# Performance work log

Measured on AMD Instinct MI355X. Metric: run time of the kernel, lower is better.

The kernel has to match this reference:

```python
import jax, jax.numpy as jnp
import numpy as np

B, L, NMOD = 200, 50, 3          # dialogues, uniform dialogue length, modalities (l,a,v)
N_DIM, NHIDDEN, NUM_K, NSPK = 128, 128, 4, 2
NN = B * NMOD * L                # total graph nodes = 30000


def _build_edge_index():
    # within-modality full permutations per dialogue
    idx = np.arange(L)
    u, v = np.meshgrid(idx, idx, indexing='ij')
    m = u != v
    pw = np.stack([u[m], v[m]])                                    # [2, L*(L-1)]
    offs = (np.arange(B)[:, None] * NMOD * L + np.arange(NMOD)[None, :] * L).reshape(-1)
    within = (pw[None, :, :] + offs[:, None, None]).transpose(1, 0, 2).reshape(2, -1)
    # cross-modal permutations of (l_t, a_t, v_t) per utterance
    mo = np.arange(NMOD) * L
    mu, mv = np.meshgrid(mo, mo, indexing='ij')
    mm = mu != mv
    pc = np.stack([mu[mm], mv[mm]])                                # [2, 6]
    offs2 = (np.arange(B)[:, None] * NMOD * L + np.arange(L)[None, :]).reshape(-1)
    cross = (pc[None, :, :] + offs2[:, None, None]).transpose(1, 0, 2).reshape(2, -1)
    return np.concatenate([within, cross], axis=1).astype(np.int32)  # [2, 1530000]


def setup_inputs():
    key = jax.random.key(0)
    ks = jax.random.split(key, 6)
    a = jax.random.normal(ks[0], (B * L, N_DIM), jnp.float32)
    v = jax.random.normal(ks[1], (B * L, N_DIM), jnp.float32)
    l = jax.random.normal(ks[2], (B * L, N_DIM), jnp.float32)
    qmask = jax.random.uniform(ks[3], (L, B, NSPK), jnp.float32)
    W1 = jax.random.normal(ks[4], (NHIDDEN, N_DIM), jnp.float32) / np.sqrt(N_DIM)
    b1 = jnp.zeros((NHIDDEN,), jnp.float32)
    speaker_emb = jax.random.normal(ks[5], (NSPK, N_DIM), jnp.float32)
    kappas = jnp.ones((NUM_K,), jnp.float32)
    edge_index = jnp.asarray(_build_edge_index())
    return {"a": a, "v": v, "l": l, "qmask": qmask, "W1": W1, "b1": b1,
            "speaker_emb": speaker_emb, "kappas": kappas,
            "edge_index": edge_index, "epoch": 0}


def _hgcn_block(x, src, dst, inv_deg, kappa):
    # gather-aggregate-scatter hypergraph conv: mean over incoming edges, kappa-weighted residual
    agg = jax.ops.segment_sum(x[src], dst, num_segments=NN) * inv_deg
    return jax.nn.relu(x + kappa * agg)


def reference(a, v, l, qmask, W1, b1, speaker_emb, kappas, edge_index, epoch):
    # flatten qmask per dialogue (uniform lengths) -> speaker id per utterance
    spk_idx = jnp.argmax(qmask.transpose(1, 0, 2).reshape(B * L, NSPK), axis=-1)
    l = l + speaker_emb[spk_idx]                    # use_speaker and 'l' in modals
    # per-dialogue node ordering: [l_b; a_b; v_b]
    feats = jnp.concatenate([l.reshape(B, L, N_DIM),
                             a.reshape(B, L, N_DIM),
                             v.reshape(B, L, N_DIM)], axis=1).reshape(NN, N_DIM)
    x = feats @ W1.T + b1
    src, dst = edge_index[0], edge_index[1]
    deg = jax.ops.segment_sum(jnp.ones((src.shape[0],), jnp.float32), dst, num_segments=NN)
    inv_deg = (1.0 / jnp.maximum(deg, 1.0))[:, None]
    for k in range(NUM_K):
        x = _hgcn_block(x, src, dst, inv_deg, kappas[k])
    x = jnp.concatenate([feats, x], axis=-1)        # use_residue
    D = x.shape[-1]
    xr = x.reshape(B, NMOD, L, D)
    # reverse_features: cat l/a/v feature blocks along last dim, utterance-major
    out = jnp.concatenate([xr[:, 0], xr[:, 1], xr[:, 2]], axis=-1).reshape(B * L, NMOD * D)
    return out
```

## Files before the change

### kernel.cpp

```cpp
#include <hip/hip_runtime.h>

#define NB   200
#define LL   50
#define ND   128

typedef __attribute__((ext_vector_type(8))) short bf16x8;
typedef __attribute__((ext_vector_type(4))) float f32x4;

#define FS   136
#define SMEM_BYTES (192 * FS * 2)

__device__ __forceinline__ short f2bf(float x) {
    unsigned u = __float_as_uint(x);
    return (short)((u + 0x7fffu + ((u >> 16) & 1u)) >> 16);
}

__device__ __forceinline__ bf16x8 pack8(f32x4 lo, f32x4 hi) {
    bf16x8 r;
    r[0] = f2bf(lo[0]); r[1] = f2bf(lo[1]); r[2] = f2bf(lo[2]); r[3] = f2bf(lo[3]);
    r[4] = f2bf(hi[0]); r[5] = f2bf(hi[1]); r[6] = f2bf(hi[2]); r[7] = f2bf(hi[3]);
    return r;
}

__launch_bounds__(1024, 4)
__global__ void hgcn_fused(const float* __restrict__ a,
                           const float* __restrict__ v,
                           const float* __restrict__ l,
                           const float* __restrict__ qmask,
                           const float* __restrict__ W1,
                           const float* __restrict__ b1,
                           const float* __restrict__ se,
                           const float* __restrict__ kap,
                           float* __restrict__ out) {
    extern __shared__ char smem[];
    short* featsB = (short*)smem;

    const int b    = blockIdx.x;
    const int tid  = threadIdx.x;
    const int lane = tid & 63;
    const int w    = tid >> 6;
    const int r    = lane & 15;
    const int q    = lane >> 4;

    const f32x4* a4  = (const f32x4*)a;
    const f32x4* v4  = (const f32x4*)v;
    const f32x4* l4  = (const f32x4*)l;
    const f32x4* se4 = (const f32x4*)se;
    const f32x4* W14 = (const f32x4*)W1;
    f32x4* out4 = (f32x4*)out;

    f32x4 kap4 = {0.f, 0.f, 0.f, 0.f};
    float bias = 0.0f;
    bf16x8 wfr[4];
    const int d = 16 * w + r;
    if (tid < 512) {
        kap4 = *(const f32x4*)kap;
        bias = b1[d];
        #pragma unroll
        for (int ks = 0; ks < 4; ++ks) {
            f32x4 g0 = W14[d * 32 + ks * 8 + q * 2];
            f32x4 g1 = W14[d * 32 + ks * 8 + q * 2 + 1];
            wfr[ks] = pack8(g0, g1);
        }
    }

    for (int i = tid; i < 3072; i += 1024) {
        int prow = i >> 4, c8 = i & 15;
        int m = prow >> 6, t = prow & 63;
        f32x4 f0 = {0.f, 0.f, 0.f, 0.f}, f1 = {0.f, 0.f, 0.f, 0.f};
        if (t < LL) {
            const f32x4* src = (m == 0) ? l4 : ((m == 1) ? a4 : v4);
            int base = (b * LL + t) * 32 + c8 * 2;
            f0 = src[base]; f1 = src[base + 1];
            if (m == 0) {
                int qb  = (t * NB + b) * 2;
                int spk = qmask[qb + 1] > qmask[qb] ? 1 : 0;
                f0 += se4[spk * 32 + c8 * 2];
                f1 += se4[spk * 32 + c8 * 2 + 1];
            }
        }
        *(bf16x8*)&featsB[prow * FS + c8 * 8] = pack8(f0, f1);
    }
    __syncthreads();

    if (tid < 512) {
        f32x4 acc[12];
        #pragma unroll
        for (int nt = 0; nt < 12; ++nt) acc[nt] = (f32x4){0.f, 0.f, 0.f, 0.f};
        #pragma unroll
        for (int ks = 0; ks < 4; ++ks)
            #pragma unroll
            for (int nt = 0; nt < 12; ++nt) {
                bf16x8 af = *(const bf16x8*)&featsB[(16 * nt + r) * FS + ks * 32 + q * 8];
                acc[nt] = __builtin_amdgcn_mfma_f32_16x16x32_bf16(af, wfr[ks], acc[nt], 0, 0, 0);
            }

        #pragma unroll
        for (int nt = 0; nt < 12; ++nt) {
            int t0 = 16 * (nt & 3) + 4 * q;
            #pragma unroll
            for (int e = 0; e < 4; ++e)
                acc[nt][e] = (t0 + e < LL) ? acc[nt][e] + bias : 0.0f;
        }

        const float inv = 1.0f / 51.0f;
        #pragma unroll
        for (int it = 0; it < 4; ++it) {
            const float f = kap4[it] * inv;
            const float g = 1.0f - 2.0f * f;
            float S[3];
            #pragma unroll
            for (int m = 0; m < 3; ++m) {
                f32x4 s4 = acc[4 * m] + acc[4 * m + 1] + acc[4 * m + 2] + acc[4 * m + 3];
                float s = s4[0] + s4[1] + s4[2] + s4[3];
                s += __shfl_xor(s, 16, 64);
                s += __shfl_xor(s, 32, 64);
                S[m] = s;
            }
            #pragma unroll
            for (int j = 0; j < 4; ++j) {
                int t0 = 16 * j + 4 * q;
                #pragma unroll
                for (int e = 0; e < 4; ++e) {
                    float c = acc[j][e] + acc[4 + j][e] + acc[8 + j][e];
                    bool valid = (t0 + e) < LL;
                    #pragma unroll
                    for (int m = 0; m < 3; ++m) {
                        float xv = acc[4 * m + j][e];
                        float nv = fmaxf(fmaf(f, S[m] + c, g * xv), 0.0f);
                        acc[4 * m + j][e] = valid ? nv : 0.0f;
                    }
                }
            }
        }

        const size_t ob = (size_t)b * LL * 768 + 128 + d;
        #pragma unroll
        for (int m = 0; m < 3; ++m)
            #pragma unroll
            for (int j = 0; j < 4; ++j) {
                int t0 = 16 * j + 4 * q;
                #pragma unroll
                for (int e = 0; e < 4; ++e) {
                    int t = t0 + e;
                    if (t < LL)
                        out[ob + (size_t)t * 768 + m * 256] = acc[4 * m + j][e];
                }
            }
    } else {
        for (int i = tid - 512; i < 2400; i += 512) {
            int row = i >> 4, c8 = i & 15;
            int m = row >= 100 ? 2 : (row >= 50 ? 1 : 0);
            int t = row - m * 50;
            const f32x4* src = (m == 0) ? l4 : ((m == 1) ? a4 : v4);
            int base = (b * LL + t) * 32 + c8 * 2;
            f32x4 f0 = src[base], f1 = src[base + 1];
            if (m == 0) {
                int qb  = (t * NB + b) * 2;
                int spk = qmask[qb + 1] > qmask[qb] ? 1 : 0;
                f0 += se4[spk * 32 + c8 * 2];
                f1 += se4[spk * 32 + c8 * 2 + 1];
            }
            size_t o = (size_t)(b * LL + t) * 192 + m * 64 + c8 * 2;
            out4[o]     = f0;
            out4[o + 1] = f1;
        }
    }
}

extern "C" void kernel_launch(void* const* d_in, const int* in_sizes, int n_in,
                              void* d_out, int out_size, void* d_ws, size_t ws_size,
                              hipStream_t stream) {
    const float* a     = (const float*)d_in[0];
    const float* v     = (const float*)d_in[1];
    const float* l     = (const float*)d_in[2];
    const float* qmask = (const float*)d_in[3];
    const float* W1    = (const float*)d_in[4];
    const float* b1    = (const float*)d_in[5];
    const float* se    = (const float*)d_in[6];
    const float* kap   = (const float*)d_in[7];
    float* out = (float*)d_out;

    hipFuncSetAttribute((const void*)hgcn_fused,
                        hipFuncAttributeMaxDynamicSharedMemorySize, SMEM_BYTES);
    hgcn_fused<<<NB, 1024, SMEM_BYTES, stream>>>(a, v, l, qmask, W1, b1, se, kap, out);
}
```

Before: 17.93 us.

## Hoist global loads before barrier, use packed bf16 convert and nontemporal stores

Restructures the feature staging so each thread loads its l/a/v rows once into registers, and the second half-block prefetches its passthrough rows before the barrier instead of reloading them afterward. It also swaps the software bf16 rounding for the hardware packed conversion instruction and makes the output writes nontemporal. The goal is to overlap global load latency with the weight setup and to cut instruction count. In exchange it raises register pressure in the 1024-thread block, and the hardware conversion may round differently from the manual routine.

```diff
diff --git a/kernel.cpp b/kernel.cpp
--- a/kernel.cpp
+++ b/kernel.cpp
@@ -10,16 +10,13 @@
 #define FS   136
 #define SMEM_BYTES (192 * FS * 2)
 
-__device__ __forceinline__ short f2bf(float x) {
-    unsigned u = __float_as_uint(x);
-    return (short)((u + 0x7fffu + ((u >> 16) & 1u)) >> 16);
-}
-
 __device__ __forceinline__ bf16x8 pack8(f32x4 lo, f32x4 hi) {
-    bf16x8 r;
-    r[0] = f2bf(lo[0]); r[1] = f2bf(lo[1]); r[2] = f2bf(lo[2]); r[3] = f2bf(lo[3]);
-    r[4] = f2bf(hi[0]); r[5] = f2bf(hi[1]); r[6] = f2bf(hi[2]); r[7] = f2bf(hi[3]);
-    return r;
+    union { bf16x8 h; unsigned u[4]; } r;
+    asm("v_cvt_pk_bf16_f32 %0, %1, %2" : "=v"(r.u[0]) : "v"(lo[0]), "v"(lo[1]));
+    asm("v_cvt_pk_bf16_f32 %0, %1, %2" : "=v"(r.u[1]) : "v"(lo[2]), "v"(lo[3]));
+    asm("v_cvt_pk_bf16_f32 %0, %1, %2" : "=v"(r.u[2]) : "v"(hi[0]), "v"(hi[1]));
+    asm("v_cvt_pk_bf16_f32 %0, %1, %2" : "=v"(r.u[3]) : "v"(hi[2]), "v"(hi[3]));
+    return r.h;
 }
 
 __launch_bounds__(1024, 4)
@@ -49,10 +46,37 @@
     const f32x4* W14 = (const f32x4*)W1;
     f32x4* out4 = (f32x4*)out;
 
-    f32x4 kap4 = {0.f, 0.f, 0.f, 0.f};
+    const f32x4 z4 = {0.f, 0.f, 0.f, 0.f};
+
+    const int srow = tid >> 4;
+    const int c8   = tid & 15;
+    const bool vrow = srow < LL;
+    const int gbase = (b * LL + (vrow ? srow : 0)) * 32 + c8 * 2;
+
+    f32x4 se00 = se4[c8 * 2],      se01 = se4[c8 * 2 + 1];
+    f32x4 se10 = se4[32 + c8 * 2], se11 = se4[32 + c8 * 2 + 1];
+    f32x4 sl0 = z4, sl1 = z4, sa0 = z4, sa1 = z4, sv0 = z4, sv1 = z4;
+    float q0 = 0.f, q1 = 0.f;
+    if (vrow) {
+        sl0 = l4[gbase]; sl1 = l4[gbase + 1];
+        sa0 = a4[gbase]; sa1 = a4[gbase + 1];
+        sv0 = v4[gbase]; sv1 = v4[gbase + 1];
+        int qb = (srow * NB + b) * 2;
+        q0 = qmask[qb]; q1 = qmask[qb + 1];
+    }
+
+    f32x4 kap4 = z4;
     float bias = 0.0f;
     bf16x8 wfr[4];
     const int d = 16 * w + r;
+    f32x4 F0[5], F1[5];
+    float Q0[5], Q1[5];
+    int   MM[5], TT[5];
+    bool  VV[5];
+    const int ft  = tid - 512;
+    const int rf  = ft >> 4;
+    const int c8f = ft & 15;
+
     if (tid < 512) {
         kap4 = *(const f32x4*)kap;
         bias = b1[d];
@@ -62,31 +86,41 @@
             f32x4 g1 = W14[d * 32 + ks * 8 + q * 2 + 1];
             wfr[ks] = pack8(g0, g1);
         }
-    }
-
-    for (int i = tid; i < 3072; i += 1024) {
-        int prow = i >> 4, c8 = i & 15;
-        int m = prow >> 6, t = prow & 63;
-        f32x4 f0 = {0.f, 0.f, 0.f, 0.f}, f1 = {0.f, 0.f, 0.f, 0.f};
-        if (t < LL) {
-            const f32x4* src = (m == 0) ? l4 : ((m == 1) ? a4 : v4);
-            int base = (b * LL + t) * 32 + c8 * 2;
-            f0 = src[base]; f1 = src[base + 1];
-            if (m == 0) {
-                int qb  = (t * NB + b) * 2;
-                int spk = qmask[qb + 1] > qmask[qb] ? 1 : 0;
-                f0 += se4[spk * 32 + c8 * 2];
-                f1 += se4[spk * 32 + c8 * 2 + 1];
-            }
-        }
-        *(bf16x8*)&featsB[prow * FS + c8 * 8] = pack8(f0, f1);
-    }
+    } else {
+        #pragma unroll
+        for (int k = 0; k < 5; ++k) {
+            int prow = rf + 32 * k;
+            bool val = prow < 150;
+            int m = prow >= 100 ? 2 : (prow >= 50 ? 1 : 0);
+            int t = prow - m * 50;
+            MM[k] = m; TT[k] = t; VV[k] = val;
+            Q0[k] = 0.f; Q1[k] = 0.f;
+            if (val) {
+                const f32x4* src = (m == 0) ? l4 : ((m == 1) ? a4 : v4);
+                int gb = (b * LL + t) * 32 + c8f * 2;
+                F0[k] = src[gb]; F1[k] = src[gb + 1];
+                if (m == 0) {
+                    int qb = (t * NB + b) * 2;
+                    Q0[k] = qmask[qb]; Q1[k] = qmask[qb + 1];
+                }
+            }
+        }
+    }
+
+    if (vrow) {
+        bool spk = q1 > q0;
+        sl0 += spk ? se10 : se00;
+        sl1 += spk ? se11 : se01;
+    }
+    *(bf16x8*)&featsB[srow * FS + c8 * 8]         = pack8(sl0, sl1);
+    *(bf16x8*)&featsB[(64 + srow) * FS + c8 * 8]  = pack8(sa0, sa1);
+    *(bf16x8*)&featsB[(128 + srow) * FS + c8 * 8] = pack8(sv0, sv1);
     __syncthreads();
 
     if (tid < 512) {
         f32x4 acc[12];
         #pragma unroll
-        for (int nt = 0; nt < 12; ++nt) acc[nt] = (f32x4){0.f, 0.f, 0.f, 0.f};
+        for (int nt = 0; nt < 12; ++nt) acc[nt] = z4;
         #pragma unroll
         for (int ks = 0; ks < 4; ++ks)
             #pragma unroll
@@ -144,26 +178,24 @@
                 for (int e = 0; e < 4; ++e) {
                     int t = t0 + e;
                     if (t < LL)
-                        out[ob + (size_t)t * 768 + m * 256] = acc[4 * m + j][e];
+                        __builtin_nontemporal_store(acc[4 * m + j][e],
+                                                    &out[ob + (size_t)t * 768 + m * 256]);
                 }
             }
     } else {
-        for (int i = tid - 512; i < 2400; i += 512) {
-            int row = i >> 4, c8 = i & 15;
-            int m = row >= 100 ? 2 : (row >= 50 ? 1 : 0);
-            int t = row - m * 50;
-            const f32x4* src = (m == 0) ? l4 : ((m == 1) ? a4 : v4);
-            int base = (b * LL + t) * 32 + c8 * 2;
-            f32x4 f0 = src[base], f1 = src[base + 1];
-            if (m == 0) {
-                int qb  = (t * NB + b) * 2;
-                int spk = qmask[qb + 1] > qmask[qb] ? 1 : 0;
-                f0 += se4[spk * 32 + c8 * 2];
-                f1 += se4[spk * 32 + c8 * 2 + 1];
-            }
-            size_t o = (size_t)(b * LL + t) * 192 + m * 64 + c8 * 2;
-            out4[o]     = f0;
-            out4[o + 1] = f1;
+        #pragma unroll
+        for (int k = 0; k < 5; ++k) {
+            if (VV[k]) {
+                f32x4 f0 = F0[k], f1 = F1[k];
+                if (MM[k] == 0) {
+                    bool spk = Q1[k] > Q0[k];
+                    f0 += spk ? se10 : se00;
+                    f1 += spk ? se11 : se01;
+                }
+                size_t o = (size_t)(b * LL + TT[k]) * 192 + MM[k] * 64 + c8f * 2;
+                __builtin_nontemporal_store(f0, &out4[o]);
+                __builtin_nontemporal_store(f1, &out4[o + 1]);
+            }
         }
     }
 }
```

Result: no change. 18.08 us (+0.8%).
